# Optimization experiments

Measured on AMD Instinct MI355X. Metric: run time of the kernel, lower is better.

## Reference

```python
import jax, jax.numpy as jnp
import numpy as np

N_HEADS = 8
ATT_DIM = 64


def _pos_enc(x):
    # x: (chan, L, bs, D); sinusoidal PE added along axis -3 (the query/key slot dim)
    L, D = x.shape[-3], x.shape[-1]
    pos = np.arange(L)[:, None].astype(np.float32)
    div = np.exp(np.arange(0, D, 2).astype(np.float32) * (-np.log(10000.0) / D))
    pe = np.zeros((L, 1, D), dtype=np.float32)
    pe[:, 0, 0::2] = np.sin(pos * div)
    pe[:, 0, 1::2] = np.cos(pos * div)
    return x + jnp.asarray(pe)


def setup_inputs() -> dict:
    key = jax.random.key(0)
    ks = jax.random.split(key, 6)
    C, NQ, NK, B, QD, KD = 8, 16, 32, 128, 128, 128
    E = N_HEADS * ATT_DIM  # 512
    OUT = ATT_DIM  # out_dim defaults to attention_dim
    b = np.float32(1.0 / np.sqrt(ATT_DIM))
    bp = np.float32(1.0 / np.sqrt(OUT))
    return {
        "q": jax.random.normal(ks[0], (C, NQ, B, QD), dtype=jnp.float32),
        "k": jax.random.normal(ks[1], (C, NK, B, KD), dtype=jnp.float32),
        "Wq": jax.random.uniform(ks[2], (C, NQ, QD, E), jnp.float32, -b, b),
        "Wk": jax.random.uniform(ks[3], (C, NK, KD, E), jnp.float32, -b, b),
        "Wv": jax.random.uniform(ks[4], (C, NK, KD, E), jnp.float32, -b, b),
        "Wp": jax.random.uniform(ks[5], (C, NQ, E, OUT), jnp.float32, -bp, bp),
    }


def reference(q, k, Wq, Wk, Wv, Wp):
    H, A = N_HEADS, ATT_DIM
    C, NQ, B, _ = q.shape
    NK = k.shape[1]
    inv_temp = jnp.float32(1.0 / np.sqrt(A))
    q_pe = _pos_enc(q)
    k_pe = _pos_enc(k)
    # per-channel grouped QKV projections: (C, N, B, D) x (C, N, D, E) -> (C, N, B, E)
    query = jnp.einsum('cqbd,cqde->cqbe', q_pe, Wq).reshape(C, NQ, B, H, A)
    key_t = jnp.einsum('ckbd,ckde->ckbe', k_pe, Wk).reshape(C, NK, B, H, A)
    value = jnp.einsum('ckbd,ckde->ckbe', k_pe, Wv).reshape(C, NK, B, H, A)
    # attention scores per (channel, batch, head)
    logits = jnp.einsum('cqbha,ckbha->cbhqk', query, key_t) * inv_temp
    attn = jax.nn.softmax(logits, axis=-1)
    # value aggregation (original does broadcast-multiply+sum; einsum is the same math)
    out = jnp.einsum('cbhqk,ckbha->cqbha', attn, value).reshape(C, NQ, B, H * A)
    # per-channel output projection
    return jnp.einsum('cqbe,cqeo->cqbo', out, Wp)
```

## Files before the change

### kernel.cpp

```cpp
#include <hip/hip_runtime.h>

#define C_  8
#define NQ_ 16
#define NK_ 32
#define B_  128
#define D_  128
#define E_  512
#define H_  8
#define A_  64
#define O_  64

typedef __attribute__((ext_vector_type(4))) float f32x4;
typedef __attribute__((ext_vector_type(8))) short bf16x8;
typedef __attribute__((ext_vector_type(4))) short bf16x4;

__device__ __forceinline__ short f2bf(float f) {
    union { float f; unsigned u; } v; v.f = f;
    unsigned r = v.u + 0x7fffu + ((v.u >> 16) & 1u);
    return (short)(r >> 16);
}

__global__ __launch_bounds__(256) void qkv_proj_kernel(
    const float* __restrict__ qin, const float* __restrict__ kin,
    const float* __restrict__ Wq, const float* __restrict__ Wk,
    const float* __restrict__ Wv,
    short* __restrict__ wsq, short* __restrict__ wsk, short* __restrict__ wsv)
{
    const int tid   = threadIdx.x;
    const int blk   = blockIdx.x;
    const int e_blk = blk & 3;
    const int unit  = blk >> 2;

    const float* X; const float* W; short* Y; int n; size_t ypitch;
    if (unit < C_ * NQ_) {
        const int c = unit >> 4;
        n = unit & 15;
        X = qin + (size_t)unit * B_ * D_;
        W = Wq  + (size_t)unit * D_ * E_;
        Y = wsq + (size_t)c * B_ * NQ_ * E_ + (size_t)n * E_;
        ypitch = (size_t)NQ_ * E_;
    } else if (unit < C_ * (NQ_ + NK_)) {
        const int u = unit - C_ * NQ_;
        const int c = u >> 5;
        n = u & 31;
        X = kin + (size_t)u * B_ * D_;
        W = Wk  + (size_t)u * D_ * E_;
        Y = wsk + (size_t)c * B_ * NK_ * E_ + (size_t)n * E_;
        ypitch = (size_t)NK_ * E_;
    } else {
        const int u = unit - C_ * (NQ_ + NK_);
        const int c = u >> 5;
        n = u & 31;
        X = kin + (size_t)u * B_ * D_;
        W = Wv  + (size_t)u * D_ * E_;
        Y = wsv + (size_t)c * B_ * NK_ * E_ + (size_t)n * E_;
        ypitch = (size_t)NK_ * E_;
    }

    const int wv   = tid >> 6;
    const int lane = tid & 63;
    const int lr   = lane & 15;
    const int quad = lane >> 4;
    const int wrow = (wv >> 1) * 64;
    const int wcol = (wv & 1) * 64;
    const int ecol = e_blk * 128 + wcol;

    f32x4 acc[4][4];
    #pragma unroll
    for (int m = 0; m < 4; ++m)
        #pragma unroll
        for (int nf = 0; nf < 4; ++nf)
            acc[m][nf] = (f32x4){0.f, 0.f, 0.f, 0.f};

    #pragma unroll
    for (int k0 = 0; k0 < D_; k0 += 64) {
        float peval;
        {
            const int d = k0 + lane;
            const float freq = expf((float)(d & ~1) * (-9.210340371976184f / (float)D_));
            const float arg  = (float)n * freq;
            peval = (d & 1) ? cosf(arg) : sinf(arg);
        }

        #pragma unroll
        for (int ks = 0; ks < 2; ++ks) {
            const int kc = k0 + ks * 32 + quad * 8;

            f32x4 a0[4], a1[4];
            #pragma unroll
            for (int m = 0; m < 4; ++m) {
                const float* ar = X + (size_t)(wrow + m * 16 + lr) * D_ + kc;
                a0[m] = *(const f32x4*)ar;
                a1[m] = *(const f32x4*)(ar + 4);
            }

            float bw[4][8];
            #pragma unroll
            for (int nf = 0; nf < 4; ++nf) {
                const float* br = W + (size_t)kc * E_ + ecol + nf * 16 + lr;
                #pragma unroll
                for (int j = 0; j < 8; ++j)
                    bw[nf][j] = br[(size_t)j * E_];
            }

            float pj[8];
            #pragma unroll
            for (int j = 0; j < 8; ++j)
                pj[j] = __shfl(peval, ks * 32 + quad * 8 + j);

            bf16x8 af[4], bfr[4];
            #pragma unroll
            for (int m = 0; m < 4; ++m) {
                #pragma unroll
                for (int j = 0; j < 4; ++j) {
                    af[m][j]     = f2bf(a0[m][j] + pj[j]);
                    af[m][4 + j] = f2bf(a1[m][j] + pj[4 + j]);
                }
            }
            #pragma unroll
            for (int nf = 0; nf < 4; ++nf)
                #pragma unroll
                for (int j = 0; j < 8; ++j)
                    bfr[nf][j] = f2bf(bw[nf][j]);

            #pragma unroll
            for (int m = 0; m < 4; ++m)
                #pragma unroll
                for (int nf = 0; nf < 4; ++nf)
                    acc[m][nf] = __builtin_amdgcn_mfma_f32_16x16x32_bf16(
                        af[m], bfr[nf], acc[m][nf], 0, 0, 0);
        }
    }

    #pragma unroll
    for (int m = 0; m < 4; ++m)
        #pragma unroll
        for (int nf = 0; nf < 4; ++nf)
            #pragma unroll
            for (int r = 0; r < 4; ++r) {
                const int row = wrow + m * 16 + quad * 4 + r;
                const int col = e_blk * 128 + wcol + nf * 16 + lr;
                Y[(size_t)row * ypitch + col] = f2bf(acc[m][nf][r]);
            }
}

__global__ __launch_bounds__(256) void attn_kernel(
    const short* __restrict__ wsq, const short* __restrict__ wsk,
    const short* __restrict__ wsv, short* __restrict__ wso)
{
    __shared__ __align__(16) short Ks[32][264];
    __shared__ __align__(16) short Vs[32][258];
    __shared__ __align__(16) short Ps[4][16][40];

    const int tid = threadIdx.x;
    const int pb  = blockIdx.x;
    const int b   = pb & (B_ - 1);
    const int c   = pb >> 7;

    const short* qb0 = wsq + ((size_t)(c * B_ + b) * NQ_) * E_;
    const short* kb0 = wsk + ((size_t)(c * B_ + b) * NK_) * E_;
    const short* vb0 = wsv + ((size_t)(c * B_ + b) * NK_) * E_;
    short*       ob0 = wso + ((size_t)(c * NQ_) * B_ + b) * E_;

    const int wv   = tid >> 6;
    const int lane = tid & 63;
    const int lr   = lane & 15;
    const int quad = lane >> 4;
    const int lcol = wv * 64;
    const int nloc = tid >> 5;
    const int ch   = tid & 31;

    auto loadKV = [&](const short* kb, const short* vb,
                      bf16x8 (&kr)[4], bf16x8 (&vr)[4]) {
        #pragma unroll
        for (int i = 0; i < 4; ++i)
            kr[i] = *(const bf16x8*)(kb + (size_t)(nloc + i * 8) * E_ + ch * 8);
        #pragma unroll
        for (int i = 0; i < 4; ++i)
            vr[i] = *(const bf16x8*)(vb + (size_t)(nloc + i * 8) * E_ + ch * 8);
    };
    auto writeKV = [&](bf16x8 (&kr)[4], bf16x8 (&vr)[4]) {
        #pragma unroll
        for (int i = 0; i < 4; ++i)
            *(bf16x8*)&Ks[nloc + i * 8][ch * 8] = kr[i];
        #pragma unroll
        for (int i = 0; i < 4; ++i)
            #pragma unroll
            for (int p = 0; p < 4; ++p)
                *(int*)&Vs[nloc + i * 8][ch * 8 + p * 2] = ((const int*)&vr[i])[p];
    };

    auto computeUnit = [&](const short* qb, short* ob) {
        const bf16x8 aq0 = *(const bf16x8*)(qb + (size_t)lr * E_ + lcol + quad * 8);
        const bf16x8 aq1 = *(const bf16x8*)(qb + (size_t)lr * E_ + lcol + 32 + quad * 8);

        f32x4 sacc0 = (f32x4){0.f, 0.f, 0.f, 0.f};
        f32x4 sacc1 = (f32x4){0.f, 0.f, 0.f, 0.f};
        {
            const int kc0 = lcol + quad * 8;
            sacc0 = __builtin_amdgcn_mfma_f32_16x16x32_bf16(aq0, *(const bf16x8*)&Ks[lr][kc0], sacc0, 0, 0, 0);
            sacc1 = __builtin_amdgcn_mfma_f32_16x16x32_bf16(aq0, *(const bf16x8*)&Ks[16 + lr][kc0], sacc1, 0, 0, 0);
            const int kc1 = lcol + 32 + quad * 8;
            sacc0 = __builtin_amdgcn_mfma_f32_16x16x32_bf16(aq1, *(const bf16x8*)&Ks[lr][kc1], sacc0, 0, 0, 0);
            sacc1 = __builtin_amdgcn_mfma_f32_16x16x32_bf16(aq1, *(const bf16x8*)&Ks[16 + lr][kc1], sacc1, 0, 0, 0);
        }

        float p0[4], p1[4];
        #pragma unroll
        for (int r = 0; r < 4; ++r) {
            const float v0 = sacc0[r] * 0.125f;
            const float v1 = sacc1[r] * 0.125f;
            float m = fmaxf(v0, v1);
            m = fmaxf(m, __shfl_xor(m, 1));
            m = fmaxf(m, __shfl_xor(m, 2));
            m = fmaxf(m, __shfl_xor(m, 4));
            m = fmaxf(m, __shfl_xor(m, 8));
            const float e0 = __expf(v0 - m);
            const float e1 = __expf(v1 - m);
            float s = e0 + e1;
            s += __shfl_xor(s, 1);
            s += __shfl_xor(s, 2);
            s += __shfl_xor(s, 4);
            s += __shfl_xor(s, 8);
            const float inv = 1.0f / s;
            p0[r] = e0 * inv;
            p1[r] = e1 * inv;
        }

        #pragma unroll
        for (int r = 0; r < 4; ++r) {
            Ps[wv][quad * 4 + r][lr]      = f2bf(p0[r]);
            Ps[wv][quad * 4 + r][16 + lr] = f2bf(p1[r]);
        }
        __syncthreads();
        const bf16x8 ap = *(const bf16x8*)&Ps[wv][lr][quad * 8];

        short* Osb = ((short*)Ks) + wv * 1024;

        #pragma unroll
        for (int t = 0; t < 4; ++t) {
            bf16x8 bvv;
            #pragma unroll
            for (int j = 0; j < 8; ++j)
                bvv[j] = Vs[quad * 8 + j][lcol + t * 16 + lr];
            f32x4 oacc = (f32x4){0.f, 0.f, 0.f, 0.f};
            oacc = __builtin_amdgcn_mfma_f32_16x16x32_bf16(ap, bvv, oacc, 0, 0, 0);
            #pragma unroll
            for (int r = 0; r < 4; ++r)
                Osb[(quad * 4 + r) * 64 + t * 16 + lr] = f2bf(oacc[r]);
        }

        const int q   = lane >> 2;
        const int seg = lane & 3;
        const bf16x8 oA = *(const bf16x8*)&Osb[q * 64 + seg * 16];
        const bf16x8 oB = *(const bf16x8*)&Osb[q * 64 + seg * 16 + 8];
        short* dst = ob + (size_t)q * (B_ * E_) + lcol + seg * 16;
        *(bf16x8*)dst       = oA;
        *(bf16x8*)(dst + 8) = oB;
    };

    bf16x8 kr0[4], vr0[4], kr1[4], vr1[4];
    loadKV(kb0, vb0, kr0, vr0);
    writeKV(kr0, vr0);
    __syncthreads();

    loadKV(kb0 + 256, vb0 + 256, kr1, vr1);
    computeUnit(qb0, ob0);
    __syncthreads();

    writeKV(kr1, vr1);
    __syncthreads();
    computeUnit(qb0 + 256, ob0 + 256);
}

__global__ __launch_bounds__(256) void out_proj_kernel(
    const short* __restrict__ wso, const float* __restrict__ Wp,
    float* __restrict__ out)
{
    __shared__ __align__(16) short Xlds[32 * 512];
    __shared__ __align__(16) short Wlds[32 * 512];

    const int tid = threadIdx.x;
    const int blk = blockIdx.x;
    const int cq  = blk >> 3;
    const int bh  = (blk >> 1) & 3;
    const int oh  = blk & 1;

    const short* Xb = wso + (size_t)cq * B_ * E_ + (size_t)bh * 32 * E_;
    const float* Wb = Wp  + (size_t)cq * E_ * O_ + oh * 32;
    float*       Ob = out + (size_t)cq * B_ * O_ + (size_t)bh * 32 * O_ + oh * 32;

    const int xrow = tid >> 3;
    const int xch  = tid & 7;
    const int o    = tid & 31;
    const int kg   = tid >> 5;

    bf16x8 xv[8];
    #pragma unroll
    for (int s = 0; s < 8; ++s)
        xv[s] = *(const bf16x8*)(Xb + (size_t)xrow * E_ + s * 64 + xch * 8);

    float wr[8][8];
    #pragma unroll
    for (int s = 0; s < 8; ++s)
        #pragma unroll
        for (int j = 0; j < 8; ++j)
            wr[s][j] = Wb[(size_t)(s * 64 + kg * 8 + j) * O_ + o];

    #pragma unroll
    for (int s = 0; s < 8; ++s) {
        const int g = (s * 8 + xch) ^ (xrow & 7);
        *(bf16x8*)&Xlds[xrow * 512 + g * 8] = xv[s];
    }
    #pragma unroll
    for (int s = 0; s < 8; ++s) {
        bf16x8 w8;
        #pragma unroll
        for (int j = 0; j < 8; ++j) w8[j] = f2bf(wr[s][j]);
        const int g = (s * 8 + kg) ^ (o & 7);
        *(bf16x8*)&Wlds[o * 512 + g * 8] = w8;
    }
    __syncthreads();

    const int wv   = tid >> 6;
    const int lane = tid & 63;
    const int lr   = lane & 15;
    const int quad = lane >> 4;
    const int rowh = wv >> 1;
    const int ohh  = wv & 1;
    const int arow = rowh * 16 + lr;
    const int brow = ohh * 16 + lr;

    f32x4 acc = (f32x4){0.f, 0.f, 0.f, 0.f};
    #pragma unroll
    for (int st = 0; st < 16; ++st) {
        const int ga = (st * 4 + quad) ^ (arow & 7);
        const int gb = (st * 4 + quad) ^ (brow & 7);
        const bf16x8 af  = *(const bf16x8*)&Xlds[arow * 512 + ga * 8];
        const bf16x8 bfr = *(const bf16x8*)&Wlds[brow * 512 + gb * 8];
        acc = __builtin_amdgcn_mfma_f32_16x16x32_bf16(af, bfr, acc, 0, 0, 0);
    }

    #pragma unroll
    for (int r = 0; r < 4; ++r)
        Ob[(size_t)(rowh * 16 + quad * 4 + r) * O_ + ohh * 16 + lr] = acc[r];
}

extern "C" void kernel_launch(void* const* d_in, const int* in_sizes, int n_in,
                              void* d_out, int out_size, void* d_ws, size_t ws_size,
                              hipStream_t stream) {
    const float* q  = (const float*)d_in[0];
    const float* k  = (const float*)d_in[1];
    const float* Wq = (const float*)d_in[2];
    const float* Wk = (const float*)d_in[3];
    const float* Wv = (const float*)d_in[4];
    const float* Wp = (const float*)d_in[5];
    float* out = (float*)d_out;

    const size_t sz_q = (size_t)C_ * NQ_ * B_ * E_;
    const size_t sz_k = (size_t)C_ * NK_ * B_ * E_;
    short* wsq = (short*)d_ws;
    short* wsk = wsq + sz_q;
    short* wsv = wsk + sz_k;
    short* wso = wsv + sz_k;

    qkv_proj_kernel<<<dim3(2560), dim3(256), 0, stream>>>(q, k, Wq, Wk, Wv, wsq, wsk, wsv);
    attn_kernel<<<dim3(1024), dim3(256), 0, stream>>>(wsq, wsk, wsv, wso);
    out_proj_kernel<<<dim3(1024), dim3(256), 0, stream>>>(wso, Wp, out);
}
```

Baseline: 269.9 us.

## Stage QKV projection operands through double-buffered LDS via global_load_lds

```diff
diff --git a/kernel.cpp b/kernel.cpp
--- a/kernel.cpp
+++ b/kernel.cpp
@@ -20,12 +20,21 @@
     return (short)(r >> 16);
 }
 
+__device__ __forceinline__ void gl_lds16(const float* g, float* l) {
+    __builtin_amdgcn_global_load_lds(
+        (const __attribute__((address_space(1))) void*)g,
+        (__attribute__((address_space(3))) void*)l, 16, 0, 0);
+}
+
 __global__ __launch_bounds__(256) void qkv_proj_kernel(
     const float* __restrict__ qin, const float* __restrict__ kin,
     const float* __restrict__ Wq, const float* __restrict__ Wk,
     const float* __restrict__ Wv,
     short* __restrict__ wsq, short* __restrict__ wsk, short* __restrict__ wsv)
 {
+    __shared__ __align__(16) float Abuf[2][4096];
+    __shared__ __align__(16) float Bbuf[2][4096];
+
     const int tid   = threadIdx.x;
     const int blk   = blockIdx.x;
     const int e_blk = blk & 3;
@@ -63,7 +72,43 @@
     const int quad = lane >> 4;
     const int wrow = (wv >> 1) * 64;
     const int wcol = (wv & 1) * 64;
-    const int ecol = e_blk * 128 + wcol;
+
+    const int l8   = lane >> 3;
+    const int l7   = lane & 7;
+    const int chnk = l7 >> 1;
+    const int hoff = (l7 & 1) * 4;
+    const int l32  = lane >> 5;
+    const int g31  = lane & 31;
+
+    float peA, peB;
+    {
+        const float base = -9.210340371976184f / (float)D_;
+        float freq = expf((float)(lane & ~1) * base);
+        float arg  = (float)n * freq;
+        peA = (lane & 1) ? cosf(arg) : sinf(arg);
+        const int d2 = 64 + lane;
+        freq = expf((float)(d2 & ~1) * base);
+        arg  = (float)n * freq;
+        peB = (d2 & 1) ? cosf(arg) : sinf(arg);
+    }
+
+    auto stage = [&](int bf, int s) {
+        const int k0s = s * 32;
+        #pragma unroll
+        for (int i = 0; i < 4; ++i) {
+            const int row = i * 32 + wv * 8 + l8;
+            const int cg  = chnk ^ (row & 3);
+            gl_lds16(X + (size_t)row * D_ + k0s + cg * 8 + hoff,
+                     &Abuf[bf][i * 1024 + wv * 256]);
+        }
+        #pragma unroll
+        for (int i = 0; i < 4; ++i) {
+            const int k  = i * 8 + wv * 2 + l32;
+            const int gg = g31 ^ (((k >> 3) & 3) << 1);
+            gl_lds16(W + (size_t)(k0s + k) * E_ + e_blk * 128 + gg * 4,
+                     &Bbuf[bf][i * 1024 + wv * 256]);
+        }
+    };
 
     f32x4 acc[4][4];
     #pragma unroll
@@ -72,64 +117,54 @@
         for (int nf = 0; nf < 4; ++nf)
             acc[m][nf] = (f32x4){0.f, 0.f, 0.f, 0.f};
 
-    #pragma unroll
-    for (int k0 = 0; k0 < D_; k0 += 64) {
-        float peval;
-        {
-            const int d = k0 + lane;
-            const float freq = expf((float)(d & ~1) * (-9.210340371976184f / (float)D_));
-            const float arg  = (float)n * freq;
-            peval = (d & 1) ? cosf(arg) : sinf(arg);
-        }
-
-        #pragma unroll
-        for (int ks = 0; ks < 2; ++ks) {
-            const int kc = k0 + ks * 32 + quad * 8;
-
-            f32x4 a0[4], a1[4];
-            #pragma unroll
-            for (int m = 0; m < 4; ++m) {
-                const float* ar = X + (size_t)(wrow + m * 16 + lr) * D_ + kc;
-                a0[m] = *(const f32x4*)ar;
-                a1[m] = *(const f32x4*)(ar + 4);
+    stage(0, 0);
+    __syncthreads();
+
+    #pragma unroll
+    for (int s = 0; s < 4; ++s) {
+        const int cur = s & 1;
+        if (s < 3) stage(cur ^ 1, s + 1);
+
+        float pj[8];
+        #pragma unroll
+        for (int j = 0; j < 8; ++j) {
+            const int kg = s * 32 + quad * 8 + j;
+            pj[j] = (kg < 64) ? __shfl(peA, kg) : __shfl(peB, kg - 64);
+        }
+
+        bf16x8 af[4];
+        #pragma unroll
+        for (int m = 0; m < 4; ++m) {
+            const int row = wrow + m * 16 + lr;
+            const int cg  = quad ^ (row & 3);
+            const f32x4 x0 = *(const f32x4*)&Abuf[cur][row * 32 + cg * 8];
+            const f32x4 x1 = *(const f32x4*)&Abuf[cur][row * 32 + cg * 8 + 4];
+            #pragma unroll
+            for (int j = 0; j < 4; ++j) {
+                af[m][j]     = f2bf(x0[j] + pj[j]);
+                af[m][4 + j] = f2bf(x1[j] + pj[4 + j]);
             }
-
-            float bw[4][8];
-            #pragma unroll
-            for (int nf = 0; nf < 4; ++nf) {
-                const float* br = W + (size_t)kc * E_ + ecol + nf * 16 + lr;
-                #pragma unroll
-                for (int j = 0; j < 8; ++j)
-                    bw[nf][j] = br[(size_t)j * E_];
+        }
+
+        bf16x8 bfr[4];
+        #pragma unroll
+        for (int nf = 0; nf < 4; ++nf) {
+            #pragma unroll
+            for (int j = 0; j < 8; ++j) {
+                const int kk = quad * 8 + j;
+                const int el = (wcol + nf * 16 + lr) ^ (quad << 3);
+                bfr[nf][j] = f2bf(Bbuf[cur][kk * 128 + el]);
             }
-
-            float pj[8];
-            #pragma unroll
-            for (int j = 0; j < 8; ++j)
-                pj[j] = __shfl(peval, ks * 32 + quad * 8 + j);
-
-            bf16x8 af[4], bfr[4];
-            #pragma unroll
-            for (int m = 0; m < 4; ++m) {
-                #pragma unroll
-                for (int j = 0; j < 4; ++j) {
-                    af[m][j]     = f2bf(a0[m][j] + pj[j]);
-                    af[m][4 + j] = f2bf(a1[m][j] + pj[4 + j]);
-                }
-            }
+        }
+
+        #pragma unroll
+        for (int m = 0; m < 4; ++m)
             #pragma unroll
             for (int nf = 0; nf < 4; ++nf)
-                #pragma unroll
-                for (int j = 0; j < 8; ++j)
-                    bfr[nf][j] = f2bf(bw[nf][j]);
-
-            #pragma unroll
-            for (int m = 0; m < 4; ++m)
-                #pragma unroll
-                for (int nf = 0; nf < 4; ++nf)
-                    acc[m][nf] = __builtin_amdgcn_mfma_f32_16x16x32_bf16(
-                        af[m], bfr[nf], acc[m][nf], 0, 0, 0);
-        }
+                acc[m][nf] = __builtin_amdgcn_mfma_f32_16x16x32_bf16(
+                    af[m], bfr[nf], acc[m][nf], 0, 0, 0);
+
+        __syncthreads();
     }
 
     #pragma unroll
```

Result: faster. 257.7 us (-4.5%).
